# Optimization experiments

Measured on AMD Instinct MI355X. Metric: run time of the kernel, lower is better.

Reference implementation:

```python
import jax, jax.numpy as jnp
import numpy as np
from jax import lax

DT = 0.1  # integration step, matches dt=0.1 default
B, T, N = 8, 4096, 1024


def setup_inputs() -> dict:
    key = jax.random.key(0)
    ks = jax.random.split(key, 6)
    E = jax.random.normal(ks[0], (B, T, N), dtype=jnp.float32)
    r = jax.random.uniform(ks[1], (N,), dtype=jnp.float32)            # NonNeg
    tau_nu = 1.0 + jax.random.uniform(ks[2], (N,), dtype=jnp.float32)  # NonNeg, >0
    M = jax.random.uniform(ks[3], (N,), dtype=jnp.float32)            # NonNeg
    sigma = 0.5 + jax.random.uniform(ks[4], (N,), dtype=jnp.float32)  # NonNeg, >0
    th = 0.1 * jax.random.normal(ks[5], (N,), dtype=jnp.float32)
    return {"E": E, "r": r, "tau_nu": tau_nu, "M": M, "sigma": sigma, "th": th}


def reference(E, r, tau_nu, M, sigma, th):
    """Wilson-Cowan-like rate recurrence.

    Phi(x) = M*x/(x^2+sigma^2) * relu(x+th)
    nu_{t+1} = nu_t + dt/tau_nu * (-nu_t + Phi(E_t - r*nu_t))
    E: [B,T,N]; params: [N]; returns nu trajectory [B,T,N].
    """
    def phi(x):
        return M * x / (x * x + sigma * sigma) * jax.nn.relu(x + th)

    coef = DT / tau_nu  # [N]

    def step(nu, e_t):  # nu: [B,N], e_t: [B,N]
        u = e_t - r * nu
        nu_new = nu + coef * (phi(u) - nu)
        return nu_new, nu_new

    nu0 = jnp.zeros((E.shape[0], E.shape[2]), dtype=E.dtype)
    _, outs = lax.scan(step, nu0, jnp.swapaxes(E, 0, 1))  # outs: [T,B,N]
    return jnp.swapaxes(outs, 0, 1)
```

## Files before the change

### kernel.cpp

```cpp
#include <hip/hip_runtime.h>


#define DT_STEP 0.1f

constexpr int Bc = 8;
constexpr int Tc = 4096;
constexpr int Nc = 1024;
constexpr int D  = 32;

__global__ __launch_bounds__(64, 1) void cw_recurrence_kernel(
    const float* __restrict__ E,
    const float* __restrict__ r,
    const float* __restrict__ tau_nu,
    const float* __restrict__ M,
    const float* __restrict__ sigma,
    const float* __restrict__ th,
    float* __restrict__ out)
{
    const int idx = blockIdx.x * 64 + threadIdx.x;
    const int b = idx >> 10;
    const int n = idx & (Nc - 1);

    const float rv   = r[n];
    const float coef = DT_STEP / tau_nu[n];
    const float Mv   = M[n];
    const float sv   = sigma[n];
    const float s2   = sv * sv;
    const float thv  = th[n];

    const float* lp = E   + (size_t)b * Tc * Nc + n;
    float*       sp = out + (size_t)b * Tc * Nc + n;

    float nu = 0.0f;
    float buf[D];

#pragma unroll
    for (int j = 0; j < D; ++j) {
        asm volatile("global_load_dword %0, %1, off" : "=v"(buf[j]) : "v"(lp));
        lp += Nc;
    }

#define WAITK(K, slot) asm volatile("s_waitcnt vmcnt(" #K ")" : "+v"(buf[slot]))
#define BODY(slot) do {                                                  \
        float e   = buf[slot];                                           \
        float u   = fmaf(-rv, nu, e);                                    \
        float dd  = fmaf(u, u, s2);                                      \
        float inv = __builtin_amdgcn_rcpf(dd);                           \
        float g   = fmaxf(u + thv, 0.0f);                                \
        float phi = (Mv * u) * (inv * g);                                \
        nu = fmaf(coef, phi - nu, nu);                                   \
        asm volatile("global_store_dword %0, %1, off" :: "v"(sp), "v"(nu)); \
        sp += Nc;                                                        \
    } while (0)
#define LOADQ(slot) do {                                                 \
        asm volatile("global_load_dword %0, %1, off" : "=v"(buf[slot]) : "v"(lp)); \
        lp += Nc;                                                        \
    } while (0)

#define SHEAD(j, K) WAITK(K, j); BODY(j); LOADQ(j);
#define SMAIN(j)    WAITK(62, j); BODY(j); LOADQ(j);
#define STAIL(j, K) WAITK(K, j); BODY(j);

    SHEAD(0,31)  SHEAD(1,32)  SHEAD(2,33)  SHEAD(3,34)
    SHEAD(4,35)  SHEAD(5,36)  SHEAD(6,37)  SHEAD(7,38)
    SHEAD(8,39)  SHEAD(9,40)  SHEAD(10,41) SHEAD(11,42)
    SHEAD(12,43) SHEAD(13,44) SHEAD(14,45) SHEAD(15,46)
    SHEAD(16,47) SHEAD(17,48) SHEAD(18,49) SHEAD(19,50)
    SHEAD(20,51) SHEAD(21,52) SHEAD(22,53) SHEAD(23,54)
    SHEAD(24,55) SHEAD(25,56) SHEAD(26,57) SHEAD(27,58)
    SHEAD(28,59) SHEAD(29,60) SHEAD(30,61) SHEAD(31,62)

    for (int k = 1; k <= 126; ++k) {
        SMAIN(0)  SMAIN(1)  SMAIN(2)  SMAIN(3)
        SMAIN(4)  SMAIN(5)  SMAIN(6)  SMAIN(7)
        SMAIN(8)  SMAIN(9)  SMAIN(10) SMAIN(11)
        SMAIN(12) SMAIN(13) SMAIN(14) SMAIN(15)
        SMAIN(16) SMAIN(17) SMAIN(18) SMAIN(19)
        SMAIN(20) SMAIN(21) SMAIN(22) SMAIN(23)
        SMAIN(24) SMAIN(25) SMAIN(26) SMAIN(27)
        SMAIN(28) SMAIN(29) SMAIN(30) SMAIN(31)
    }

    STAIL(0,62)  STAIL(1,61)  STAIL(2,60)  STAIL(3,59)
    STAIL(4,58)  STAIL(5,57)  STAIL(6,56)  STAIL(7,55)
    STAIL(8,54)  STAIL(9,53)  STAIL(10,52) STAIL(11,51)
    STAIL(12,50) STAIL(13,49) STAIL(14,48) STAIL(15,47)
    STAIL(16,46) STAIL(17,45) STAIL(18,44) STAIL(19,43)
    STAIL(20,42) STAIL(21,41) STAIL(22,40) STAIL(23,39)
    STAIL(24,38) STAIL(25,37) STAIL(26,36) STAIL(27,35)
    STAIL(28,34) STAIL(29,33) STAIL(30,32) STAIL(31,31)

#undef WAITK
#undef BODY
#undef LOADQ
#undef SHEAD
#undef SMAIN
#undef STAIL
}

extern "C" void kernel_launch(void* const* d_in, const int* in_sizes, int n_in,
                              void* d_out, int out_size, void* d_ws, size_t ws_size,
                              hipStream_t stream) {
    const float* E      = (const float*)d_in[0];
    const float* r      = (const float*)d_in[1];
    const float* tau_nu = (const float*)d_in[2];
    const float* M      = (const float*)d_in[3];
    const float* sigma  = (const float*)d_in[4];
    const float* th     = (const float*)d_in[5];
    float* out = (float*)d_out;

    const int total = Bc * Nc;
    const int block = 64;
    const int grid  = total / block;

    cw_recurrence_kernel<<<grid, block, 0, stream>>>(E, r, tau_nu, M, sigma, th, out);
}
```

Baseline: 306.2 us.

## Use buffer loads/stores with scalar offsets and fold coef into phi update

Replaces the global_load/store instructions, which carry per-lane 64-bit address registers, with buffer_load/store using a resource descriptor, a fixed per-lane voffset and an advancing scalar soffset. This removes the per-step 64-bit vector pointer arithmetic. The recurrence is also rewritten algebraically by folding coef into M and using (1-coef)*nu, which takes a subtraction and a multiply off the serial dependency chain. The byte offset is 32-bit, so b*Tc*Nc*4 (up to ~128MB) must fit, and the rounding differs slightly from before.

New measurement: 309.1 us. Within noise of the previous version (+1.0%).

```diff
diff --git a/kernel.cpp b/kernel.cpp
--- a/kernel.cpp
+++ b/kernel.cpp
@@ -7,6 +7,18 @@
 constexpr int Tc = 4096;
 constexpr int Nc = 1024;
 constexpr int D  = 32;
+
+typedef int v4i __attribute__((ext_vector_type(4)));
+
+__device__ __forceinline__ v4i make_srd(const void* p) {
+    union { const void* p; unsigned long long u; } a; a.p = p;
+    v4i r;
+    r.x = (int)(a.u & 0xFFFFFFFFull);
+    r.y = (int)((a.u >> 32) & 0xFFFFull);
+    r.z = (int)0xFFFFFFFFu;
+    r.w = 0x00020000;
+    return r;
+}
 
 __global__ __launch_bounds__(64, 1) void cw_recurrence_kernel(
     const float* __restrict__ E,
@@ -23,38 +35,44 @@
 
     const float rv   = r[n];
     const float coef = DT_STEP / tau_nu[n];
-    const float Mv   = M[n];
+    const float cM   = coef * M[n];
+    const float omc  = 1.0f - coef;
     const float sv   = sigma[n];
     const float s2   = sv * sv;
     const float thv  = th[n];
 
-    const float* lp = E   + (size_t)b * Tc * Nc + n;
-    float*       sp = out + (size_t)b * Tc * Nc + n;
+    const v4i rsE = make_srd(E);
+    const v4i rsO = make_srd(out);
+    const unsigned int voff = (unsigned int)((b * Tc * Nc + n) * 4);
+    unsigned int soL = 0;
+    unsigned int soS = 0;
 
     float nu = 0.0f;
     float buf[D];
 
 #pragma unroll
     for (int j = 0; j < D; ++j) {
-        asm volatile("global_load_dword %0, %1, off" : "=v"(buf[j]) : "v"(lp));
-        lp += Nc;
+        asm volatile("buffer_load_dword %0, %1, %2, %3 offen"
+                     : "=v"(buf[j]) : "v"(voff), "s"(rsE), "s"(soL));
+        soL += Nc * 4;
     }
 
 #define WAITK(K, slot) asm volatile("s_waitcnt vmcnt(" #K ")" : "+v"(buf[slot]))
-#define BODY(slot) do {                                                  \
-        float e   = buf[slot];                                           \
-        float u   = fmaf(-rv, nu, e);                                    \
-        float dd  = fmaf(u, u, s2);                                      \
-        float inv = __builtin_amdgcn_rcpf(dd);                           \
-        float g   = fmaxf(u + thv, 0.0f);                                \
-        float phi = (Mv * u) * (inv * g);                                \
-        nu = fmaf(coef, phi - nu, nu);                                   \
-        asm volatile("global_store_dword %0, %1, off" :: "v"(sp), "v"(nu)); \
-        sp += Nc;                                                        \
+#define BODY(slot) do {                                                   \
+        float u   = fmaf(-rv, nu, buf[slot]);                             \
+        float dd  = fmaf(u, u, s2);                                       \
+        float inv = __builtin_amdgcn_rcpf(dd);         \
+        float g   = fmaxf(u + thv, 0.0f);           \
+        float cp  = (cM * u) * g;                                         \
+        nu = fmaf(cp, inv, omc * nu);                                     \
+        asm volatile("buffer_store_dword %0, %1, %2, %3 offen"            \
+                     :: "v"(nu), "v"(voff), "s"(rsO), "s"(soS));          \
+        soS += Nc * 4;                                                    \
     } while (0)
-#define LOADQ(slot) do {                                                 \
-        asm volatile("global_load_dword %0, %1, off" : "=v"(buf[slot]) : "v"(lp)); \
-        lp += Nc;                                                        \
+#define LOADQ(slot) do {                                                  \
+        asm volatile("buffer_load_dword %0, %1, %2, %3 offen"             \
+                     : "=v"(buf[slot]) : "v"(voff), "s"(rsE), "s"(soL));  \
+        soL += Nc * 4;                                                    \
     } while (0)
 
 #define SHEAD(j, K) WAITK(K, j); BODY(j); LOADQ(j);
```
